# Optimization experiments

Hardware: AMD Instinct MI355X
Metric: run time of the kernel (lower is better)

Reference implementation:

```python
import jax, jax.numpy as jnp
from jax import lax
import numpy as np

D_MODEL = 2048
NUM_EXPERTS = 16
NUM_TOKENS = 8192  # must be divisible by NUM_EXPERTS (balanced assignment)


def setup_inputs() -> dict:
    key = jax.random.key(0)
    k1, k2 = jax.random.split(key)
    features = jax.random.normal(k1, (NUM_TOKENS, D_MODEL), dtype=jnp.float32)
    # gate weight (orthogonal init in torch; gaussian is fine for a numerical baseline)
    W = jax.random.normal(k2, (NUM_EXPERTS, D_MODEL), dtype=jnp.float32) * 0.1
    b = jnp.zeros((NUM_EXPERTS,), dtype=jnp.float32)
    return {"features": features, "W": W, "b": b, "is_training": 1}


def _balanced_assignment(scores):
    """Greedy balanced assignment: each expert receives exactly T//E tokens.
    Deterministic stand-in for the cpp auction-based balanced_assignment: scan
    over tokens, each token takes its best-scoring expert with remaining capacity.
    Returns sort_by_expert: token indices sorted (stably) by assigned expert."""
    T, E = scores.shape
    cap_per_expert = T // E

    def step(cap, s):  # cap: [E] remaining capacity, s: [E] token's scores
        masked = jnp.where(cap > 0, s, -jnp.inf)
        e = jnp.argmax(masked)
        return cap.at[e].add(-1), e

    _, tok2exp = lax.scan(step, jnp.full((E,), cap_per_expert, dtype=jnp.int32), scores)
    sort_by_expert = jnp.argsort(tok2exp, stable=True)  # [T] token ids grouped by expert
    return sort_by_expert


def reference(features, W, b, is_training):
    # gating computed under no_grad in the original
    affinities = lax.stop_gradient(features @ W.T + b)  # [T, E]
    T, E = affinities.shape
    cap = T // E

    sort_by_expert = _balanced_assignment(affinities)

    routing_probs = jax.nn.softmax(affinities, axis=1)  # [T, E]

    # gather_scores: permute probs into expert order, pick each token's score for
    # its assigned expert, then un-permute back to original token order.
    sorted_probs = routing_probs[sort_by_expert]                 # [T, E]
    expert_idx = (jnp.arange(T) // cap)[:, None]                 # [T, 1], balanced splits
    gathered = jnp.take_along_axis(sorted_probs, expert_idx, axis=1)  # [T, 1]
    i_sort = jnp.argsort(sort_by_expert)                         # inverse permutation
    gathered_scores = gathered[i_sort]                           # [T, 1]

    return sort_by_expert, gathered_scores
```

## Files before the change

kernel.cpp:

```cpp
#include <hip/hip_runtime.h>
#include <hip/hip_bf16.h>
#include <math.h>

#define T_TOK 8192
#define D_MODEL 2048
#define N_EXP 16
#define CAP 512
#define NSEG (T_TOK / 64)


__device__ __forceinline__ unsigned int f2ord(float f) {
    unsigned int b = __float_as_uint(f);
    return (b & 0x80000000u) ? ~b : (b | 0x80000000u);
}

__global__ __launch_bounds__(256, 4) void gemm_aff_kernel(
    const float* __restrict__ feat, const float* __restrict__ W,
    float* __restrict__ aff)
{
    const int tid  = threadIdx.x;
    const int wave = tid >> 6, lane = tid & 63;
    const int tbase = blockIdx.x * 16 + wave * 4;

    const float* fbase = feat + (size_t)tbase * D_MODEL + lane * 4;

    float acc[64];
    #pragma unroll
    for (int i = 0; i < 64; ++i) acc[i] = 0.f;

    float4 cur[4], nxt[4];
    #pragma unroll
    for (int r = 0; r < 4; ++r)
        cur[r] = *(const float4*)(fbase + (size_t)r * D_MODEL);

    #pragma unroll
    for (int j = 0; j < 8; ++j) {
        if (j < 7) {
            #pragma unroll
            for (int r = 0; r < 4; ++r)
                nxt[r] = *(const float4*)(fbase + (size_t)r * D_MODEL + (j + 1) * 256);
        }
        const float* wbase = W + j * 256 + lane * 4;
        #pragma unroll
        for (int g = 0; g < 4; ++g) {
            float4 wv[4];
            #pragma unroll
            for (int i = 0; i < 4; ++i)
                wv[i] = *(const float4*)(wbase + (size_t)(g * 4 + i) * D_MODEL);
            #pragma unroll
            for (int i = 0; i < 4; ++i)
                #pragma unroll
                for (int r = 0; r < 4; ++r) {
                    acc[r * 16 + g * 4 + i] += cur[r].x * wv[i].x;
                    acc[r * 16 + g * 4 + i] += cur[r].y * wv[i].y;
                    acc[r * 16 + g * 4 + i] += cur[r].z * wv[i].z;
                    acc[r * 16 + g * 4 + i] += cur[r].w * wv[i].w;
                }
        }
        #pragma unroll
        for (int r = 0; r < 4; ++r) cur[r] = nxt[r];
    }

    #pragma unroll
    for (int step = 0; step < 6; ++step) {
        const int m    = 1 << step;
        const int half = 64 >> (step + 1);
        const bool hi  = (lane & m) != 0;
        #pragma unroll
        for (int jj = 0; jj < half; ++jj) {
            float send = hi ? acc[jj] : acc[jj + half];
            float recv = __shfl_xor(send, m, 64);
            acc[jj] = (hi ? acc[jj + half] : acc[jj]) + recv;
        }
    }
    const int slot = ((lane & 1) << 5) | (((lane >> 1) & 1) << 4) | (((lane >> 2) & 1) << 3)
                   | (((lane >> 3) & 1) << 2) | (((lane >> 4) & 1) << 1) | ((lane >> 5) & 1);
    const int r = slot >> 4, e = slot & 15;
    aff[(size_t)(tbase + r) * N_EXP + e] = acc[0];
}

__global__ __launch_bounds__(256) void finalize_kernel(
    const float* __restrict__ aff_in, const float* __restrict__ bias,
    unsigned long long* __restrict__ pref, float* __restrict__ probs)
{
    const int t = blockIdx.x * 256 + threadIdx.x;

    float aff[N_EXP];
    const float4* p = (const float4*)(aff_in + (size_t)t * N_EXP);
    #pragma unroll
    for (int q = 0; q < 4; ++q) {
        float4 v = p[q];
        aff[q*4+0] = v.x; aff[q*4+1] = v.y; aff[q*4+2] = v.z; aff[q*4+3] = v.w;
    }
    #pragma unroll
    for (int e = 0; e < N_EXP; ++e) aff[e] += bias[e];

    float m = aff[0];
    #pragma unroll
    for (int e = 1; e < N_EXP; ++e) m = fmaxf(m, aff[e]);
    float s = 0.f;
    #pragma unroll
    for (int e = 0; e < N_EXP; ++e) s += __expf(aff[e] - m);

    float4* pr = (float4*)(probs + (size_t)t * N_EXP);
    #pragma unroll
    for (int q = 0; q < 4; ++q) {
        float4 v;
        v.x = __expf(aff[q*4+0] - m) / s;
        v.y = __expf(aff[q*4+1] - m) / s;
        v.z = __expf(aff[q*4+2] - m) / s;
        v.w = __expf(aff[q*4+3] - m) / s;
        pr[q] = v;
    }

    unsigned long long key[N_EXP];
    #pragma unroll
    for (int j = 0; j < N_EXP; ++j)
        key[j] = ((unsigned long long)f2ord(aff[j]) << 4) | (unsigned long long)(15 - j);
    unsigned long long pk = 0ull;
    unsigned int used = 0;
    for (int r = 0; r < N_EXP; ++r) {
        unsigned long long bk = 0ull; int be = 0;
        for (int j = 0; j < N_EXP; ++j)
            if (!((used >> j) & 1u) && key[j] > bk) { bk = key[j]; be = j; }
        used |= (1u << be);
        pk = (pk << 4) | (unsigned long long)be;
    }
    pref[t] = pk;
}

__global__ __launch_bounds__(512) void events_kernel(
    const unsigned long long* __restrict__ pref, int* __restrict__ evt)
{
    __shared__ unsigned long long prefL[T_TOK];
    __shared__ unsigned long long segmask[N_EXP][NSEG + 1];
    __shared__ int pseg[N_EXP][NSEG + 1];
    __shared__ int rem_cap[N_EXP], fparr[N_EXP];
    __shared__ int s_avail, s_pmin, s_fe, s_seglo;
    __shared__ int evp[N_EXP], evf[N_EXP];

    const int tid  = threadIdx.x;
    const int wave = tid >> 6, lane = tid & 63;
    const unsigned long long lt_mask = (1ull << lane) - 1ull;

    for (int i = tid; i < T_TOK; i += 512) prefL[i] = pref[i];
    if (tid < N_EXP) rem_cap[tid] = CAP;
    if (tid == 0) { s_avail = 0xFFFF; s_seglo = 0; }
    __syncthreads();

    for (int s = wave; s < NSEG; s += 8) {
        int c = (int)(prefL[s * 64 + lane] >> 60);
        #pragma unroll
        for (int e = 0; e < N_EXP; ++e) {
            unsigned long long mm = __ballot(c == e);
            if (lane == e) segmask[e][s] = mm;
        }
    }
    __syncthreads();

    for (int round = 0; round < N_EXP; ++round) {
        const unsigned int avail = (unsigned int)s_avail;

        #pragma unroll
        for (int ee = 0; ee < 2; ++ee) {
            const int e = wave + ee * 8;
            const unsigned long long m0 = segmask[e][lane];
            const unsigned long long m1 = segmask[e][64 + lane];
            const int c0 = (int)__popcll(m0), c1 = (int)__popcll(m1);
            int v0 = c0;
            #pragma unroll
            for (int d = 1; d < 64; d <<= 1) {
                int o = __shfl_up(v0, d, 64);
                if (lane >= d) v0 += o;
            }
            const int excl0 = v0 - c0;
            const int tot0  = __shfl(v0, 63, 64);
            int v1 = c1;
            #pragma unroll
            for (int d = 1; d < 64; d <<= 1) {
                int o = __shfl_up(v1, d, 64);
                if (lane >= d) v1 += o;
            }
            const int excl1 = tot0 + v1 - c1;
            pseg[e][lane]      = excl0;
            pseg[e][64 + lane] = excl1;

            int fp = 0x7FFFFFFF;
            if ((avail >> e) & 1u) {
                const int need = rem_cap[e];
                int segc = -1, kk = 0;
                if (excl0 < need && excl0 + c0 >= need)      { segc = lane;      kk = need - excl0; }
                else if (excl1 < need && excl1 + c1 >= need) { segc = 64 + lane; kk = need - excl1; }
                unsigned long long b = __ballot(segc >= 0);
                if (b) {
                    int l2    = __builtin_ctzll(b);
                    int sstar = __shfl(segc, l2, 64);
                    int k2    = __shfl(kk,   l2, 64);
                    unsigned long long m = segmask[e][sstar];
                    int rr = (int)__popcll(m & lt_mask);
                    bool hit = ((m >> lane) & 1ull) && (rr == k2 - 1);
                    unsigned long long hb = __ballot(hit);
                    fp = sstar * 64 + __builtin_ctzll(hb);
                }
            }
            if (lane == 0) fparr[e] = fp;
        }
        __syncthreads();

        if (tid == 0) {
            int pm = 0x7FFFFFFF, f = 0;
            #pragma unroll
            for (int e = 0; e < N_EXP; ++e)
                if (fparr[e] < pm) { pm = fparr[e]; f = e; }
            s_pmin = pm; s_fe = f;
        }
        __syncthreads();
        const int pmin = s_pmin, fe = s_fe;
        const int segF = pmin >> 6;
        const int seglo = s_seglo;

        if (tid < N_EXP) {
            const int e = tid;
            unsigned long long mlep = ((pmin & 63) == 63) ? ~0ull
                                      : ((1ull << ((pmin & 63) + 1)) - 1ull);
            unsigned long long m = segmask[e][segF];
            rem_cap[e] -= pseg[e][segF] + (int)__popcll(m & mlep);
            segmask[e][segF] = m & ~mlep;
        }
        for (int i = tid; i < (segF - seglo) * N_EXP; i += 512)
            segmask[i & 15][seglo + (i >> 4)] = 0ull;
        if (tid == 0) {
            evp[round] = pmin; evf[round] = fe;
            s_avail = (int)(avail & ~(1u << fe));
            s_seglo = segF;
        }
        __syncthreads();

        if (round < N_EXP - 1) {
            const unsigned int navail = avail & ~(1u << fe);
            for (int s = segF + wave; s < NSEG; s += 8) {
                unsigned long long m = segmask[fe][s];
                if (m) {
                    if ((m >> lane) & 1ull) {
                        unsigned long long pp = prefL[s * 64 + lane];
                        int e2 = (int)(pp >> 60);
                        while (!((navail >> e2) & 1u)) { pp <<= 4; e2 = (int)(pp >> 60); }
                        atomicOr(&segmask[e2][s], 1ull << lane);
                    }
                    if (lane == 0) segmask[fe][s] = 0ull;
                }
            }
        }
        __syncthreads();
    }

    if (tid < N_EXP) { evt[tid] = evp[tid]; evt[N_EXP + tid] = evf[tid]; }
}

__global__ __launch_bounds__(256) void choice_kernel(
    const unsigned long long* __restrict__ pref, const int* __restrict__ evt,
    unsigned char* __restrict__ t2e, int* __restrict__ bcnt)
{
    __shared__ int evp[N_EXP], evf[N_EXP];
    __shared__ int sc[4][N_EXP];
    const int tid = threadIdx.x, b = blockIdx.x;
    const int wave = tid >> 6, lane = tid & 63;
    if (tid < N_EXP) evp[tid] = evt[tid];
    else if (tid < 2 * N_EXP) evf[tid - N_EXP] = evt[tid];
    __syncthreads();

    const int t = b * 256 + tid;
    unsigned int mask = 0xFFFFu;
    #pragma unroll
    for (int j = 0; j < N_EXP; ++j)
        if (evp[j] < t) mask &= ~(1u << evf[j]);

    unsigned long long pp = pref[t];
    int e = (int)(pp >> 60);
    while (!((mask >> e) & 1u)) { pp <<= 4; e = (int)(pp >> 60); }
    t2e[t] = (unsigned char)e;

    #pragma unroll
    for (int e2 = 0; e2 < N_EXP; ++e2) {
        unsigned long long mm = __ballot(e == e2);
        if (lane == e2) sc[wave][e2] = (int)__popcll(mm);
    }
    __syncthreads();
    if (tid < N_EXP)
        bcnt[b * N_EXP + tid] = sc[0][tid] + sc[1][tid] + sc[2][tid] + sc[3][tid];
}

__global__ __launch_bounds__(256) void writeout_kernel(
    const unsigned char* __restrict__ t2e, const int* __restrict__ bcnt,
    const float* __restrict__ probs,
    float* __restrict__ out0, float* __restrict__ out1)
{
    __shared__ int base[N_EXP];
    __shared__ int sc[4][N_EXP];
    const int tid = threadIdx.x, b = blockIdx.x;
    const int wave = tid >> 6, lane = tid & 63;
    const unsigned long long lt_mask = (1ull << lane) - 1ull;

    const int t = b * 256 + tid;
    const int c = (int)t2e[t];

    unsigned long long own = 0ull;
    #pragma unroll
    for (int e2 = 0; e2 < N_EXP; ++e2) {
        unsigned long long mm = __ballot(c == e2);
        if (c == e2) own = mm;
        if (lane == e2) sc[wave][e2] = (int)__popcll(mm);
    }
    if (tid < N_EXP) {
        int s = 0;
        for (int b2 = 0; b2 < b; ++b2) s += bcnt[b2 * N_EXP + tid];
        base[tid] = s;
    }
    __syncthreads();

    int rank = (int)__popcll(own & lt_mask);
    for (int w2 = 0; w2 < wave; ++w2) rank += sc[w2][c];
    const int pos = base[c] + rank;
    out0[c * CAP + pos] = (float)t;
    out1[t] = probs[(size_t)t * N_EXP + c];
}

extern "C" void kernel_launch(void* const* d_in, const int* in_sizes, int n_in,
                              void* d_out, int out_size, void* d_ws, size_t ws_size,
                              hipStream_t stream) {
    const float* feat = (const float*)d_in[0];
    const float* W    = (const float*)d_in[1];
    const float* bias = (const float*)d_in[2];

    float* out = (float*)d_out;
    char*  ws  = (char*)d_ws;

    float* aff               = (float*)ws;
    unsigned long long* pref = (unsigned long long*)(ws + 524288);
    float* probs             = (float*)(ws + 589824);
    int* evt                 = (int*)(ws + 1114112);
    unsigned char* t2e       = (unsigned char*)(ws + 1114240);
    int* bcnt                = (int*)(ws + 1122432);

    hipLaunchKernelGGL(gemm_aff_kernel, dim3(512), dim3(256), 0, stream,
                       feat, W, aff);
    hipLaunchKernelGGL(finalize_kernel, dim3(T_TOK / 256), dim3(256), 0, stream,
                       aff, bias, pref, probs);
    hipLaunchKernelGGL(events_kernel, dim3(1), dim3(512), 0, stream,
                       pref, evt);
    hipLaunchKernelGGL(choice_kernel, dim3(T_TOK / 256), dim3(256), 0, stream,
                       pref, evt, t2e, bcnt);
    hipLaunchKernelGGL(writeout_kernel, dim3(T_TOK / 256), dim3(256), 0, stream,
                       t2e, bcnt, probs, out, out + T_TOK);
}
```

Before: 191.6 us.

## Stage gate weights in double-buffered LDS and serialize per-segment redistribution per thread

The affinity GEMM now loads W chunks cooperatively into a double-buffered shared-memory tile and reads them from LDS, instead of each wave reading W from global memory. This adds a barrier per chunk, and the occupancy hint drops from 4 to 2 blocks. In the balanced-assignment rounds, each thread now owns one segment and walks its set bits serially with plain ORs, replacing wave-per-segment atomicOr redistribution. The aim is to cut atomic and wave-scheduling overhead, at the cost of serial per-thread loops.

```diff
diff --git a/kernel.cpp b/kernel.cpp
--- a/kernel.cpp
+++ b/kernel.cpp
@@ -14,49 +14,73 @@
     return (b & 0x80000000u) ? ~b : (b | 0x80000000u);
 }
 
-__global__ __launch_bounds__(256, 4) void gemm_aff_kernel(
+__global__ __launch_bounds__(256, 2) void gemm_aff_kernel(
     const float* __restrict__ feat, const float* __restrict__ W,
     float* __restrict__ aff)
 {
+    __shared__ float w_lds[2][N_EXP][256];
+
     const int tid  = threadIdx.x;
     const int wave = tid >> 6, lane = tid & 63;
     const int tbase = blockIdx.x * 16 + wave * 4;
 
+    const int se  = tid >> 6;
+    const int sc4 = tid & 63;
+
     const float* fbase = feat + (size_t)tbase * D_MODEL + lane * 4;
 
     float acc[64];
     #pragma unroll
     for (int i = 0; i < 64; ++i) acc[i] = 0.f;
+
+    float4 wreg[4];
+    #pragma unroll
+    for (int q = 0; q < 4; ++q)
+        wreg[q] = *(const float4*)(W + (size_t)(q * 4 + se) * D_MODEL + sc4 * 4);
+    #pragma unroll
+    for (int q = 0; q < 4; ++q)
+        *(float4*)&w_lds[0][q * 4 + se][sc4 * 4] = wreg[q];
+    #pragma unroll
+    for (int q = 0; q < 4; ++q)
+        wreg[q] = *(const float4*)(W + (size_t)(q * 4 + se) * D_MODEL + 256 + sc4 * 4);
 
     float4 cur[4], nxt[4];
     #pragma unroll
     for (int r = 0; r < 4; ++r)
         cur[r] = *(const float4*)(fbase + (size_t)r * D_MODEL);
 
+    __syncthreads();
+
     #pragma unroll
     for (int j = 0; j < 8; ++j) {
+        const int buf = j & 1;
         if (j < 7) {
             #pragma unroll
             for (int r = 0; r < 4; ++r)
                 nxt[r] = *(const float4*)(fbase + (size_t)r * D_MODEL + (j + 1) * 256);
         }
-        const float* wbase = W + j * 256 + lane * 4;
-        #pragma unroll
-        for (int g = 0; g < 4; ++g) {
-            float4 wv[4];
-            #pragma unroll
-            for (int i = 0; i < 4; ++i)
-                wv[i] = *(const float4*)(wbase + (size_t)(g * 4 + i) * D_MODEL);
-            #pragma unroll
-            for (int i = 0; i < 4; ++i)
+        #pragma unroll
+        for (int e = 0; e < N_EXP; ++e) {
+            float4 wv = *(const float4*)&w_lds[buf][e][lane * 4];
+            #pragma unroll
+            for (int r = 0; r < 4; ++r) {
+                acc[r * 16 + e] += cur[r].x * wv.x;
+                acc[r * 16 + e] += cur[r].y * wv.y;
+                acc[r * 16 + e] += cur[r].z * wv.z;
+                acc[r * 16 + e] += cur[r].w * wv.w;
+            }
+        }
+        if (j < 7) {
+            #pragma unroll
+            for (int q = 0; q < 4; ++q)
+                *(float4*)&w_lds[buf ^ 1][q * 4 + se][sc4 * 4] = wreg[q];
+            if (j < 6) {
                 #pragma unroll
-                for (int r = 0; r < 4; ++r) {
-                    acc[r * 16 + g * 4 + i] += cur[r].x * wv[i].x;
-                    acc[r * 16 + g * 4 + i] += cur[r].y * wv[i].y;
-                    acc[r * 16 + g * 4 + i] += cur[r].z * wv[i].z;
-                    acc[r * 16 + g * 4 + i] += cur[r].w * wv[i].w;
-                }
-        }
+                for (int q = 0; q < 4; ++q)
+                    wreg[q] = *(const float4*)(W + (size_t)(q * 4 + se) * D_MODEL + (j + 2) * 256 + sc4 * 4);
+            }
+        }
+        __syncthreads();
         #pragma unroll
         for (int r = 0; r < 4; ++r) cur[r] = nxt[r];
     }
@@ -237,17 +261,19 @@
         __syncthreads();
 
         if (round < N_EXP - 1) {
-            const unsigned int navail = avail & ~(1u << fe);
-            for (int s = segF + wave; s < NSEG; s += 8) {
+            const unsigned int navail = (unsigned int)s_avail;
+            const int s = segF + tid;
+            if (s < NSEG) {
                 unsigned long long m = segmask[fe][s];
                 if (m) {
-                    if ((m >> lane) & 1ull) {
-                        unsigned long long pp = prefL[s * 64 + lane];
+                    segmask[fe][s] = 0ull;
+                    while (m) {
+                        int i = __builtin_ctzll(m); m &= m - 1ull;
+                        unsigned long long pp = prefL[s * 64 + i];
                         int e2 = (int)(pp >> 60);
                         while (!((navail >> e2) & 1u)) { pp <<= 4; e2 = (int)(pp >> 60); }
-                        atomicOr(&segmask[e2][s], 1ull << lane);
+                        segmask[e2][s] |= (1ull << i);
                     }
-                    if (lane == 0) segmask[fe][s] = 0ull;
                 }
             }
         }
```

Result: slower. 201.5 us (+5.2%).
